# Optimization experiments

Hardware: AMD Instinct MI355X
Metric: run time of the kernel (lower is better)

## Reference

```python
import jax, jax.numpy as jnp
import numpy as np

NEG = -1e9
NP_N, EP = 30000, 480000
NL, EL, T = 48, 144, 96
NA, D = 11, 256
I_STOP = NL
PHI = 1 + 5 * D + 4 * NA
VAL_VEC = jnp.array([4., 1., 3., 1., 2., 1., 5., 1., 6., 1., 1000.], dtype=jnp.float32)
BOND_VAL = jnp.array([1., 2., 3., 1.5], dtype=jnp.float32)


def gcn2(x, src, dst, w, W1, b1, W2, b2):
    # two-layer GCN with symmetric norm + self loops (PyG GCNConv semantics)
    n = x.shape[0]
    loops = jnp.arange(n, dtype=src.dtype)
    s = jnp.concatenate([src, loops])
    d = jnp.concatenate([dst, loops])
    ww = jnp.concatenate([w, jnp.ones((n,), x.dtype)])
    deg = jax.ops.segment_sum(ww, d, num_segments=n)
    dinv = jnp.where(deg > 0, deg ** -0.5, 0.0)
    norm = (ww * dinv[s] * dinv[d])[:, None]
    def conv(h, W, b):
        return jax.ops.segment_sum((h @ W)[s] * norm, d, num_segments=n) + b
    return conv(jax.nn.relu(conv(x, W1, b1)), W2, b2)


def _forward(x_p, x_l_geom, Wp1, bp1, Wp2, bp2, Wl1, bl1, Wl2, bl2,
             Wd1, bd1, Wd2, bd2, Wf, bf, Wg, bg, Wh, bh,
             src_p, dst_p, src_l, dst_l, x_l_label, bfs_index, bfs_bond):
    f32, i32 = jnp.float32, jnp.int32
    src_p = src_p.astype(i32); dst_p = dst_p.astype(i32)
    src_l = src_l.astype(i32); dst_l = dst_l.astype(i32)
    bfs_index = bfs_index.astype(i32); bfs_bond = bfs_bond.astype(i32)
    x_l_label = x_l_label.astype(i32)
    x_l = jnp.concatenate([x_l_geom, jax.nn.one_hot(x_l_label, NA, dtype=f32)], 1)
    z_pocket = gcn2(x_p, src_p, dst_p, jnp.ones((EP,), f32), Wp1, bp1, Wp2, bp2).mean(0)
    z_l = gcn2(x_l, src_l, dst_l, jnp.ones((EL,), f32), Wl1, bl1, Wl2, bl2)
    lab_true = x_l[:, 4:]
    # f: atom label classifier, teacher-forced log prob of true labels
    lmask = jnp.zeros((NA,), f32).at[-1].set(NEG)
    logp = jax.nn.log_softmax(z_l @ Wf + bf + lmask, -1)[jnp.arange(NL), x_l_label].sum()
    H_init = jnp.concatenate([z_l, lab_true], 1).mean(0)
    lab_v = jnp.concatenate([lab_true, jax.nn.one_hot(jnp.array([NA - 1]), NA, dtype=f32)], 0)  # append Stop node
    e0 = bfs_index[0]
    z_v0 = gcn2(lab_v, e0[:1], e0[1:2], jnp.ones((1,), f32), Wd1, bd1, Wd2, bd2)
    H_t0 = jnp.concatenate([z_v0, lab_v], 1).mean(0)
    val0 = lab_v @ VAL_VEC
    N1 = NL + 1
    E = 2 * T
    Q0 = jnp.zeros((T + 1,), i32).at[0].set(bfs_index[0, 0])
    carry0 = (jnp.asarray(0.0, f32), val0, jnp.zeros((N1,), bool), jnp.zeros((N1, N1), bool),
              jnp.zeros((E,), i32), jnp.zeros((E,), i32), jnp.zeros((E,), bool), jnp.asarray(0, i32),
              Q0, jnp.asarray(0, i32), jnp.asarray(1, i32), z_v0, H_t0, jnp.asarray(0.0, f32))

    def step(carry, xs):
        logp, val, closed, adj, esrc, edst, evalid, ec, Q, head, tail, z_v, H_t, time = carry
        v, bidx = xs
        active = tail > head
        u = Q[head]
        phi = jnp.concatenate([
            jnp.full((N1, 1), time, f32),
            jnp.broadcast_to(z_pocket, (N1, D)),
            jnp.broadcast_to(z_v[u], (N1, D)),
            jnp.broadcast_to(lab_v[u], (N1, NA)),
            z_v, lab_v,
            jnp.broadcast_to(H_t, (N1, D + NA)),
            jnp.broadcast_to(H_init, (N1, D + NA))], 1)
        # node mask (valency / closed / already-bonded / self), then unmask {v, stop}
        base = jnp.where((val < 1) | closed | adj[u], NEG, 0.0).at[u].set(NEG)
        m_nou = jnp.where(val[u] < 1, jnp.full((N1,), NEG, f32), base)
        m = m_nou.at[v].set(0.0).at[I_STOP].set(0.0)
        glog = (phi @ Wg + bg)[:, 0] + m
        logp = logp + jnp.where(active, jax.nn.log_softmax(glog)[v], 0.0)
        is_stop = v == I_STOP
        pop = active & is_stop
        do_edge = active & (~is_stop)
        closed = closed.at[u].set(jnp.where(pop, True, closed[u]))
        head = head + pop.astype(jnp.int32)
        Q = Q.at[tail].set(jnp.where(do_edge, v, Q[tail]), mode='drop')
        tail = tail + do_edge.astype(jnp.int32)
        esrc = esrc.at[ec].set(u, mode='drop').at[ec + 1].set(v, mode='drop')
        edst = edst.at[ec].set(v, mode='drop').at[ec + 1].set(u, mode='drop')
        evalid = evalid.at[ec].set(do_edge, mode='drop').at[ec + 1].set(do_edge, mode='drop')
        ec = ec + 2 * do_edge.astype(jnp.int32)
        # bond mask row on min valency of (u, v)
        mv = jnp.minimum(val[u], val[v])
        two = jnp.array([0., 0., NEG, 0.], f32)
        one = jnp.array([0., NEG, NEG, 0.], f32)
        zer = jnp.full((4,), NEG, f32)
        e = jnp.where(mv <= 2, two, jnp.zeros((4,), f32))
        e = jnp.where(mv <= 1, one, e)
        e = jnp.where(mv <= 0, zer, e)
        e = jnp.where(m_nou[v] <= NEG * 0.5, zer, e)
        e = e.at[bidx].set(0.0)  # unmask true bond
        hlog = phi[v] @ Wh + bh + e
        logp = logp + jnp.where(do_edge, jax.nn.log_softmax(hlog)[bidx], 0.0)
        dec = jnp.where(do_edge, BOND_VAL[bidx], 0.0)
        val = val.at[u].add(-dec).at[v].add(-dec)
        adj = adj.at[u, v].set(jnp.where(do_edge, True, adj[u, v])).at[v, u].set(jnp.where(do_edge, True, adj[v, u]))
        z_new = gcn2(lab_v, esrc, edst, evalid.astype(f32), Wd1, bd1, Wd2, bd2)
        z_v = jnp.where(do_edge, z_new, z_v)
        H_t = jnp.where(do_edge, jnp.concatenate([z_new, lab_v], 1).mean(0), H_t)
        time = time + do_edge.astype(f32)
        return (logp, val, closed, adj, esrc, edst, evalid, ec, Q, head, tail, z_v, H_t, time), None

    carry, _ = jax.lax.scan(step, carry0, (bfs_index[:, 1], bfs_bond))
    return carry[0]


def setup_inputs():
    key = jax.random.key(0)
    ks = jax.random.split(key, 30)
    f32 = jnp.float32
    def w(i, shape):
        return jax.random.normal(ks[i], shape, f32) * 0.05
    inp = {}
    inp['x_p'] = jax.random.normal(ks[0], (NP_N, 15), f32)
    inp['src_p'] = jax.random.randint(ks[1], (EP,), 0, NP_N)
    inp['dst_p'] = jax.random.randint(ks[2], (EP,), 0, NP_N)
    inp['x_l_geom'] = jax.random.normal(ks[3], (NL, 4), f32)
    inp['x_l_label'] = jax.random.randint(ks[4], (NL,), 0, NA - 1)
    inp['src_l'] = jax.random.randint(ks[5], (EL,), 0, NL)
    inp['dst_l'] = jax.random.randint(ks[6], (EL,), 0, NL)
    inp['bfs_index'] = jax.random.randint(ks[7], (T, 2), 0, NL + 1)
    inp['bfs_bond'] = jax.random.randint(ks[8], (T,), 0, 4)
    inp['Wp1'] = w(9, (15, D)); inp['bp1'] = w(10, (D,))
    inp['Wp2'] = w(11, (D, D)); inp['bp2'] = w(12, (D,))
    inp['Wl1'] = w(13, (15, D)); inp['bl1'] = w(14, (D,))
    inp['Wl2'] = w(15, (D, D)); inp['bl2'] = w(16, (D,))
    inp['Wd1'] = w(17, (NA, D)); inp['bd1'] = w(18, (D,))
    inp['Wd2'] = w(19, (D, D)); inp['bd2'] = w(20, (D,))
    inp['Wf'] = w(21, (D, NA)); inp['bf'] = w(22, (NA,))
    inp['Wg'] = w(23, (PHI, 1)); inp['bg'] = w(24, (1,))
    inp['Wh'] = w(25, (PHI, 4)); inp['bh'] = w(26, (4,))
    return inp


def reference(x_p, src_p, dst_p, x_l_geom, x_l_label, src_l, dst_l, bfs_index, bfs_bond,
              Wp1, bp1, Wp2, bp2, Wl1, bl1, Wl2, bl2, Wd1, bd1, Wd2, bd2,
              Wf, bf, Wg, bg, Wh, bh):
    return _forward(x_p, x_l_geom, Wp1, bp1, Wp2, bp2, Wl1, bl1, Wl2, bl2,
                    Wd1, bd1, Wd2, bd2, Wf, bf, Wg, bg, Wh, bh,
                    src_p, dst_p, src_l, dst_l, x_l_label, bfs_index, bfs_bond)
```

## Files before the change

kernel.cpp:

```cpp
#include <hip/hip_runtime.h>
#include <math.h>

#define NPn 30000
#define EPn 480000
#define NLl 48
#define ELl 144
#define Tn 96
#define NAn 11
#define Dn 256
#define N1 49
#define NEGf (-1000000000.0f)
#define NSTATES 97
#define CHN 125
#define PC 13
#define YN (N1*PC)


__global__ void k_deg(const int* __restrict__ dst, int* __restrict__ deg){
  int e = blockIdx.x*blockDim.x + threadIdx.x;
  if (e < EPn) atomicAdd(&deg[dst[e]], 1);
}


__global__ __launch_bounds__(256) void k_mega(
    const int* __restrict__ src_p, const int* __restrict__ dst_p, const float* __restrict__ xp,
    const int* __restrict__ deg, float* __restrict__ xagg, float* __restrict__ odegw,
    const int* __restrict__ lab_in, const int* __restrict__ bfs_i, const int* __restrict__ bfs_b,
    int* __restrict__ lab_idx, float* __restrict__ lab_means,
    int* __restrict__ dirs, int* __restrict__ dird, float* __restrict__ m_arr,
    float* __restrict__ e_arr, int* __restrict__ rec, int* __restrict__ Sout,
    const float* __restrict__ xg, const int* __restrict__ srcl, const int* __restrict__ dstl,
    const float* __restrict__ Wl1, const float* __restrict__ bl1,
    const float* __restrict__ Wl2, const float* __restrict__ bl2, float* __restrict__ zl_mean,
    const float* __restrict__ Wd2, const float* __restrict__ Wg, const float* __restrict__ Wh,
    float* __restrict__ Pm){
  const int bid = blockIdx.x;
  const int tid = threadIdx.x;

  if (bid >= 66){
    int g = (bid-66)*256 + tid;
    int e = g>>4, c = g&15;
    if (e >= EPn) return;
    int s = src_p[e], d = dst_p[e];
    if (c < 15){
      float dvs = rsqrtf((float)(deg[s]+1));
      atomicAdd(&xagg[d*16+c], xp[s*15+c]*dvs);
    } else {
      float dvd = rsqrtf((float)(deg[d]+1));
      atomicAdd(&odegw[s], dvd);
    }
    return;
  }

  if (bid == 0){
    __shared__ int sv[Tn], sb[Tn];
    __shared__ int qarr[Tn+1];
    __shared__ int2 ctrl[Tn];
    __shared__ float valuA[Tn], valvA[Tn];
    __shared__ float baseB[Tn][N1];
    __shared__ int slab[N1];
    __shared__ int cntL[NAn];
    if (tid < Tn){ sv[tid]=bfs_i[2*tid+1]; sb[tid]=bfs_b[tid]; }
    if (tid <= Tn) qarr[tid]=0;
    if (tid < NAn) cntL[tid]=0;
    if (tid < N1){ int l=(tid<NLl)? lab_in[tid] : (NAn-1); slab[tid]=l; lab_idx[tid]=l; }
    __syncthreads();
    if (tid < NLl) atomicAdd(&cntL[slab[tid]],1);
    if (tid == 0) qarr[0]=bfs_i[0];
    __syncthreads();
    if (tid < NAn){
      int c=cntL[tid];
      lab_means[tid]     = ((float)c + ((tid==NAn-1)?1.f:0.f))*(1.0f/49.0f);
      lab_means[NAn+tid] = (float)c*(1.0f/48.0f);
    }
    if (tid == 0){
      dirs[192]=qarr[0]; dird[192]=bfs_i[1];
      int head=0, tail=1, ec=0, timec=0;
      for (int t=0;t<Tn;t++){
        int v = sv[t], bix = sb[t];
        int active = (tail>head)?1:0;
        int h = (head<=Tn)? head : Tn;
        int u = qarr[h];
        int is_stop = (v==NLl)?1:0;
        int pop = active & is_stop;
        int doe = active & (is_stop^1);
        ctrl[t] = make_int2(u | (doe<<8) | (pop<<9) | (active<<10) | (timec<<16), v | (bix<<8));
        if (doe){
          if (tail<=Tn) qarr[tail]=v;
          if (ec<192){ dirs[ec]=u; dird[ec]=v; dirs[ec+1]=v; dird[ec+1]=u; }
        }
        head+=pop; tail+=doe; ec+=2*doe; timec+=doe;
      }
      Sout[0]=ec/2;
    }
    __syncthreads();
    if (tid < Tn){
      int2 c=ctrl[tid];
      rec[tid]=c.x&255; rec[Tn+tid]=c.y&255; rec[2*Tn+tid]=(c.y>>8)&3;
      rec[3*Tn+tid]=(c.x>>10)&1; rec[4*Tn+tid]=(c.x>>8)&1; rec[5*Tn+tid]=(c.x>>16)&255;
    }
    __syncthreads();
    if (tid < 64){
      const int l = tid;
      int labv = (l<N1)? slab[l] : (NAn-1);
      float val;
      switch(labv){
        case 0: val=4.f; break; case 1: val=1.f; break; case 2: val=3.f; break;
        case 3: val=1.f; break; case 4: val=2.f; break; case 5: val=1.f; break;
        case 6: val=5.f; break; case 7: val=1.f; break; case 8: val=6.f; break;
        case 9: val=1.f; break; default: val=1000.f; break;
      }
      if (l>=N1) val=0.f;
      int closed=0;
      unsigned long long adjm=0ull;
      #pragma unroll 4
      for (int t=0;t<Tn;t++){
        int2 c=ctrl[t];
        int u=c.x&255, doe=(c.x>>8)&1, pop=(c.x>>9)&1;
        int v=c.y&255, bix=(c.y>>8)&3;
        float base = (val<1.f || closed || ((adjm>>u)&1ull)) ? NEGf : 0.f;
        if (l==u) base=NEGf;
        if (l<N1) baseB[t][l]=base;
        if (l==u) valuA[t]=val;
        if (l==v) valvA[t]=val;
        if (doe){
          float dec = (bix==0)?1.f:(bix==1)?2.f:(bix==2)?3.f:1.5f;
          if (l==u){ val-=dec; adjm |= (1ull<<v); }
          if (l==v){ val-=dec; adjm |= (1ull<<u); }
        }
        if (pop && l==u) closed=1;
      }
    }
    __syncthreads();
    {
      const int lane=tid&63, wv=tid>>6;
      for (int t=wv; t<Tn; t+=4){
        float valu=valuA[t], valv=valvA[t];
        int v=sv[t], bix=sb[t];
        if (lane<N1){
          float mnou = (valu<1.f)? NEGf : baseB[t][lane];
          float m = mnou;
          if (lane==v) m=0.f;
          if (lane==NLl) m=0.f;
          m_arr[t*N1+lane]=m;
        }
        if (lane<4){
          float mnv = (valu<1.f)? NEGf : baseB[t][v];
          float mv = fminf(valu,valv);
          float e;
          if (mv<=0.f) e=NEGf;
          else if (mv<=1.f) e=((lane==1)||(lane==2))?NEGf:0.f;
          else if (mv<=2.f) e=(lane==2)?NEGf:0.f;
          else e=0.f;
          if (mnv <= NEGf*0.5f) e=NEGf;
          if (lane==bix) e=0.f;
          e_arr[t*4+lane]=e;
        }
      }
    }
    return;
  }

  if (bid == 1){
    __shared__ float sW[15*Dn];
    __shared__ __align__(16) float sagg[NLl][16];
    __shared__ float ow[NLl];
    __shared__ float rs[Dn];
    __shared__ float sdinv[NLl];
    __shared__ int sdeg[NLl];
    __shared__ int ses[ELl], sed[ELl];
    __shared__ int slab2[NLl];
    if (tid<NLl){ sdeg[tid]=1; slab2[tid]=lab_in[tid]; }
    for (int i=tid;i<NLl*16;i+=256) sagg[i>>4][i&15]=0.f;
    for (int i=tid;i<15*Dn;i+=256) sW[i]=Wl1[i];
    __syncthreads();
    if (tid<ELl){ ses[tid]=srcl[tid]; sed[tid]=dstl[tid]; atomicAdd(&sdeg[dstl[tid]],1); }
    __syncthreads();
    if (tid<NLl) sdinv[tid]=rsqrtf((float)sdeg[tid]);
    __syncthreads();
    if (tid<NLl){
      float dv=sdinv[tid];
      ow[tid]=dv;
      for (int q=0;q<4;q++) sagg[tid][q]=xg[tid*4+q]*dv;
      sagg[tid][4+slab2[tid]]=dv;
    }
    __syncthreads();
    if (tid<ELl){
      int s=ses[tid], d=sed[tid];
      float dvs=sdinv[s];
      for (int q=0;q<4;q++) atomicAdd(&sagg[d][q], xg[s*4+q]*dvs);
      atomicAdd(&sagg[d][4+slab2[s]], dvs);
      atomicAdd(&ow[s], sdinv[d]);
    }
    __syncthreads();
    {
      int c=tid;
      float wcol[16];
      #pragma unroll
      for (int q=0;q<15;q++) wcol[q]=sW[q*Dn+c];
      wcol[15]=0.f;
      float b=bl1[c];
      float rsum=0.f;
      for (int d=0;d<NLl;d++){
        const float4* ar=(const float4*)sagg[d];
        float4 x0=ar[0],x1=ar[1],x2=ar[2],x3=ar[3];
        float a=0.f;
        a=fmaf(x0.x,wcol[0],a); a=fmaf(x0.y,wcol[1],a); a=fmaf(x0.z,wcol[2],a); a=fmaf(x0.w,wcol[3],a);
        a=fmaf(x1.x,wcol[4],a); a=fmaf(x1.y,wcol[5],a); a=fmaf(x1.z,wcol[6],a); a=fmaf(x1.w,wcol[7],a);
        a=fmaf(x2.x,wcol[8],a); a=fmaf(x2.y,wcol[9],a); a=fmaf(x2.z,wcol[10],a); a=fmaf(x2.w,wcol[11],a);
        a=fmaf(x3.x,wcol[12],a); a=fmaf(x3.y,wcol[13],a); a=fmaf(x3.z,wcol[14],a);
        float h=fmaxf(sdinv[d]*a + b, 0.f);
        rsum = fmaf(sdinv[d]*ow[d], h, rsum);
      }
      rs[c]=rsum*(1.0f/48.0f);
    }
    __syncthreads();
    {
      int c=tid;
      float a=0.f;
      for (int k=0;k<Dn;k++) a=fmaf(rs[k], Wl2[(size_t)k*Dn+c], a);
      zl_mean[c]=a+bl2[c];
    }
    return;
  }

  {
    const int lane = tid&63, wv = tid>>6;
    const int k = (bid-2)*4 + wv;
    float pg=0.f;
    float4 pu=make_float4(0,0,0,0), pv=make_float4(0,0,0,0), ph=make_float4(0,0,0,0);
    for (int q=0;q<4;q++){
      int n = lane + 64*q;
      float w = Wd2[(size_t)k*Dn+n];
      pg = fmaf(w, Wg[524+n], pg);
      float4 a=*(const float4*)&Wh[(size_t)(257+n)*4];
      float4 b=*(const float4*)&Wh[(size_t)(524+n)*4];
      float4 c=*(const float4*)&Wh[(size_t)(791+n)*4];
      pu.x=fmaf(w,a.x,pu.x); pu.y=fmaf(w,a.y,pu.y); pu.z=fmaf(w,a.z,pu.z); pu.w=fmaf(w,a.w,pu.w);
      pv.x=fmaf(w,b.x,pv.x); pv.y=fmaf(w,b.y,pv.y); pv.z=fmaf(w,b.z,pv.z); pv.w=fmaf(w,b.w,pv.w);
      ph.x=fmaf(w,c.x,ph.x); ph.y=fmaf(w,c.y,ph.y); ph.z=fmaf(w,c.z,ph.z); ph.w=fmaf(w,c.w,ph.w);
    }
    for (int off=32; off>0; off>>=1){
      pg += __shfl_xor(pg,off);
      pu.x+=__shfl_xor(pu.x,off); pu.y+=__shfl_xor(pu.y,off); pu.z+=__shfl_xor(pu.z,off); pu.w+=__shfl_xor(pu.w,off);
      pv.x+=__shfl_xor(pv.x,off); pv.y+=__shfl_xor(pv.y,off); pv.z+=__shfl_xor(pv.z,off); pv.w+=__shfl_xor(pv.w,off);
      ph.x+=__shfl_xor(ph.x,off); ph.y+=__shfl_xor(ph.y,off); ph.z+=__shfl_xor(ph.z,off); ph.w+=__shfl_xor(ph.w,off);
    }
    if (lane==0){
      float* o = Pm + k*PC;
      o[0]=pg; o[1]=pu.x; o[2]=pu.y; o[3]=pu.z; o[4]=pu.w;
      o[5]=pv.x; o[6]=pv.y; o[7]=pv.z; o[8]=pv.w;
      o[9]=ph.x; o[10]=ph.y; o[11]=ph.z; o[12]=ph.w;
    }
    return;
  }
}


__global__ __launch_bounds__(256) void k_fuse(const float* __restrict__ xp, const float* __restrict__ xagg,
    const int* __restrict__ deg, const float* __restrict__ odegw,
    const float* __restrict__ Wp1, const float* __restrict__ bp1, float* __restrict__ zr){
  __shared__ float sx[CHN][16];
  __shared__ float sc[CHN];
  int tid = threadIdx.x;
  int base = blockIdx.x*CHN;
  float wcol[15];
  for (int k=0;k<15;k++) wcol[k]=Wp1[k*Dn+tid];
  float b = bp1[tid];
  for (int i=tid;i<CHN*16;i+=256){
    int n = base+(i>>4), c = i&15;
    float v = 0.f;
    if (n<NPn && c<15){
      float dv = rsqrtf((float)(deg[n]+1));
      v = (xagg[n*16+c] + xp[n*15+c]*dv)*dv;
    }
    sx[i>>4][i&15]=v;
  }
  for (int i=tid;i<CHN;i+=256){
    int n = base+i;
    float dv = (n<NPn)? rsqrtf((float)(deg[n]+1)) : 0.f;
    sc[i] = (n<NPn)? dv*(odegw[n]+dv) : 0.f;
  }
  __syncthreads();
  float acc = 0.f;
  int lim = (NPn-base < CHN)? (NPn-base) : CHN;
  for (int i=0;i<lim;i++){
    float d0 = b;
    for (int k=0;k<15;k++) d0 = fmaf(sx[i][k], wcol[k], d0);
    acc = fmaf(sc[i], fmaxf(d0,0.f), acc);
  }
  atomicAdd(&zr[tid], acc);
}


__global__ __launch_bounds__(256) void k_dcp(const int* __restrict__ Sp, const int* __restrict__ dirs,
    const int* __restrict__ dird, const int* __restrict__ lab_idx,
    const float* __restrict__ Wd1, const float* __restrict__ bd1,
    const float* __restrict__ Pm, const int* __restrict__ rec,
    const float* __restrict__ m_arr, const float* __restrict__ e_arr,
    const float* __restrict__ Wg, const float* __restrict__ Wh,
    float* __restrict__ spart){
  int k = blockIdx.x;
  if (k > Sp[0]) return;
  __shared__ float sW[11*Dn];
  __shared__ float sP[Dn*PC];
  __shared__ float hT[Dn*N1];
  __shared__ float cnt[N1*11];
  __shared__ float y1[YN];
  __shared__ float za[YN];
  __shared__ float sdinv[N1];
  __shared__ int sdeg[N1];
  __shared__ int se[192], sd[192];
  __shared__ int slab[N1];
  __shared__ int srec[6*Tn];
  int tid=threadIdx.x;
  int ecnt = (k==0)?1:(2*k);
  int base = (k==0)?192:0;
  if (tid<N1){ sdeg[tid]=1; slab[tid]=lab_idx[tid]; }
  for (int i=tid;i<N1*11;i+=256) cnt[i]=0.f;
  for (int i=tid;i<11*Dn;i+=256) sW[i]=Wd1[i];
  for (int i=tid;i<Dn*PC;i+=256) sP[i]=Pm[i];
  for (int i=tid;i<6*Tn;i+=256) srec[i]=rec[i];
  __syncthreads();
  if (tid<ecnt){ se[tid]=dirs[base+tid]; sd[tid]=dird[base+tid]; atomicAdd(&sdeg[sd[tid]],1); }
  __syncthreads();
  if (tid<N1) sdinv[tid]=rsqrtf((float)sdeg[tid]);
  __syncthreads();
  if (tid<N1) cnt[tid*11+slab[tid]] = sdinv[tid];
  __syncthreads();
  if (tid<ecnt) atomicAdd(&cnt[sd[tid]*11+slab[se[tid]]], sdinv[se[tid]]);
  __syncthreads();
  {
    int c=tid;
    float wreg[11];
    for (int a=0;a<11;a++) wreg[a]=sW[a*Dn+c];
    float b=bd1[c];
    for (int r=0;r<N1;r++){
      float s=0.f;
      for (int a=0;a<11;a++) s=fmaf(cnt[r*11+a], wreg[a], s);
      hT[c*N1+r]=fmaxf(sdinv[r]*s + b, 0.f);
    }
  }
  __syncthreads();
  for (int idx=tid; idx<YN; idx+=256){
    int r=idx/PC, j=idx-r*PC;
    float acc=0.f;
    for (int c=0;c<Dn;c++) acc=fmaf(hT[c*N1+r], sP[c*PC+j], acc);
    y1[idx]=acc;
    za[idx]=sdinv[r]*acc;
  }
  __syncthreads();
  for (int i=tid; i<ecnt*PC; i+=256){
    int e=i/PC, j=i-e*PC;
    atomicAdd(&za[sd[e]*PC+j], sdinv[se[e]]*y1[se[e]*PC+j]);
  }
  __syncthreads();
  for (int idx=tid; idx<YN; idx+=256){
    int r=idx/PC;
    za[idx]=sdinv[r]*za[idx];
  }
  __syncthreads();
  if (tid>=64) return;
  const int lane=tid;
  for (int t=0;t<Tn;t++){
    if (!srec[3*Tn+t] || srec[5*Tn+t]!=k) continue;
    const int u=srec[t], v=srec[Tn+t], doe=srec[4*Tn+t];
    float g = -INFINITY;
    float4 hm = make_float4(0,0,0,0);
    if (lane<N1){
      const float* zrow = za + lane*PC;
      g = zrow[0] + Wg[780+slab[lane]] + m_arr[t*N1+lane];
      hm.x=zrow[9]; hm.y=zrow[10]; hm.z=zrow[11]; hm.w=zrow[12];
    }
    float gv = __shfl(g, v);
    float gM = g;
    for (int off=32; off>0; off>>=1) gM = fmaxf(gM, __shfl_xor(gM, off));
    float ex = (lane<N1)? expf(g-gM) : 0.f;
    float gS = ex;
    for (int off=32; off>0; off>>=1){
      gS += __shfl_xor(gS, off);
      hm.x+=__shfl_xor(hm.x,off); hm.y+=__shfl_xor(hm.y,off);
      hm.z+=__shfl_xor(hm.z,off); hm.w+=__shfl_xor(hm.w,off);
    }
    if (lane==0){
      spart[t*5] = gv - gM - logf(gS);
      if (doe){
        const int lu=slab[u], lv=slab[v];
        const float tf=(float)k;
        for (int j=0;j<4;j++){
          float hmj = (j==0)?hm.x:(j==1)?hm.y:(j==2)?hm.z:hm.w;
          spart[t*5+1+j] = tf*Wh[j] + Wh[(513+lu)*4+j] + Wh[(780+lv)*4+j]
               + za[u*PC+1+j] + za[v*PC+5+j] + hmj*(1.0f/49.0f) + e_arr[4*t+j];
        }
      }
    }
  }
}


__global__ __launch_bounds__(256) void k_final(const float* __restrict__ zr, const float* __restrict__ Wp2,
    const float* __restrict__ bp2, const float* __restrict__ zl, const float* __restrict__ lm,
    const float* __restrict__ b2, const float* __restrict__ Wh, const float* __restrict__ bh,
    const int* __restrict__ rec, const float* __restrict__ spart, float* __restrict__ out){
  __shared__ float sr[Dn];
  __shared__ float zp[Dn];
  __shared__ float hc4s[4];
  __shared__ float red[Tn];
  int tid=threadIdx.x;
  sr[tid]=zr[tid]*(1.0f/30000.0f);
  __syncthreads();
  float a=0.f;
  for (int k=0;k<Dn;k++) a=fmaf(sr[k],Wp2[(size_t)k*Dn+tid],a);
  zp[tid]=a+bp2[tid];
  __syncthreads();
  if (tid<64){
    int lane=tid;
    float4 h=make_float4(0,0,0,0);
    for (int q=0;q<4;q++){
      int n=lane+64*q;
      float4 w1=*(const float4*)&Wh[(size_t)(1+n)*4];
      float4 w2=*(const float4*)&Wh[(size_t)(1058+n)*4];
      float4 wu=*(const float4*)&Wh[(size_t)(257+n)*4];
      float4 wv=*(const float4*)&Wh[(size_t)(524+n)*4];
      float4 wh=*(const float4*)&Wh[(size_t)(791+n)*4];
      float zpn=zp[n], zln=zl[n], bn=b2[n];
      h.x += zpn*w1.x + zln*w2.x + bn*(wu.x+wv.x+wh.x);
      h.y += zpn*w1.y + zln*w2.y + bn*(wu.y+wv.y+wh.y);
      h.z += zpn*w1.z + zln*w2.z + bn*(wu.z+wv.z+wh.z);
      h.w += zpn*w1.w + zln*w2.w + bn*(wu.w+wv.w+wh.w);
    }
    if (lane<NAn){
      float4 wa=*(const float4*)&Wh[(size_t)(1047+lane)*4];
      float4 wb=*(const float4*)&Wh[(size_t)(1314+lane)*4];
      float aa=lm[lane], bb=lm[NAn+lane];
      h.x += aa*wa.x + bb*wb.x; h.y += aa*wa.y + bb*wb.y;
      h.z += aa*wa.z + bb*wb.z; h.w += aa*wa.w + bb*wb.w;
    }
    for (int off=32; off>0; off>>=1){
      h.x+=__shfl_xor(h.x,off); h.y+=__shfl_xor(h.y,off);
      h.z+=__shfl_xor(h.z,off); h.w+=__shfl_xor(h.w,off);
    }
    if (lane==0){
      hc4s[0]=h.x+bh[0]; hc4s[1]=h.y+bh[1]; hc4s[2]=h.z+bh[2]; hc4s[3]=h.w+bh[3];
    }
  }
  __syncthreads();
  if (tid<Tn){
    int t=tid;
    float res=0.f;
    if (rec[3*Tn+t]){
      res = spart[t*5];
      if (rec[4*Tn+t]){
        int bidx = rec[2*Tn+t];
        float h0=spart[t*5+1]+hc4s[0];
        float h1=spart[t*5+2]+hc4s[1];
        float h2=spart[t*5+3]+hc4s[2];
        float h3=spart[t*5+4]+hc4s[3];
        float M=fmaxf(fmaxf(h0,h1),fmaxf(h2,h3));
        float se2=expf(h0-M)+expf(h1-M)+expf(h2-M)+expf(h3-M);
        float hb=(bidx==0)?h0:(bidx==1)?h1:(bidx==2)?h2:h3;
        res += hb - M - logf(se2);
      }
    }
    red[t]=res;
  }
  __syncthreads();
  if (tid==0){
    float s=0.f;
    for (int t=0;t<Tn;t++) s+=red[t];
    out[0]=s;
  }
}


extern "C" void kernel_launch(void* const* d_in, const int* in_sizes, int n_in,
                              void* d_out, int out_size, void* d_ws, size_t ws_size,
                              hipStream_t stream){
  const float* x_p      =(const float*)d_in[0];
  const int*   src_p    =(const int*)d_in[1];
  const int*   dst_p    =(const int*)d_in[2];
  const float* x_l_geom =(const float*)d_in[3];
  const int*   x_l_label=(const int*)d_in[4];
  const int*   src_l    =(const int*)d_in[5];
  const int*   dst_l    =(const int*)d_in[6];
  const int*   bfs_index=(const int*)d_in[7];
  const int*   bfs_bond =(const int*)d_in[8];
  const float* Wp1=(const float*)d_in[9];
  const float* bp1=(const float*)d_in[10];
  const float* Wp2=(const float*)d_in[11];
  const float* bp2=(const float*)d_in[12];
  const float* Wl1=(const float*)d_in[13];
  const float* bl1=(const float*)d_in[14];
  const float* Wl2=(const float*)d_in[15];
  const float* bl2=(const float*)d_in[16];
  const float* Wd1=(const float*)d_in[17];
  const float* bd1=(const float*)d_in[18];
  const float* Wd2=(const float*)d_in[19];
  const float* bd2=(const float*)d_in[20];
  const float* Wg =(const float*)d_in[23];
  const float* Wh =(const float*)d_in[25];
  const float* bh =(const float*)d_in[26];

  char* w=(char*)d_ws;
  size_t off=0;
  auto alloc=[&](size_t bytes)->char*{ char* p=w+off; off=(off+bytes+255)&~((size_t)255); return p; };
  int*   deg    =(int*)alloc((size_t)NPn*4);
  float* odegw  =(float*)alloc((size_t)NPn*4);
  float* xagg   =(float*)alloc((size_t)NPn*16*4);
  float* zr     =(float*)alloc(Dn*4);
  size_t zero_span = off;
  float* zl_mean=(float*)alloc(Dn*4);
  float* Pm     =(float*)alloc(Dn*PC*4);
  float* m_arr  =(float*)alloc((size_t)Tn*N1*4);
  float* e_arr  =(float*)alloc((size_t)Tn*4*4);
  int*   rec    =(int*)alloc((size_t)6*Tn*4);
  int*   dirs   =(int*)alloc(194*4);
  int*   dird   =(int*)alloc(194*4);
  int*   lab_idx=(int*)alloc(N1*4);
  float* lab_means=(float*)alloc(2*NAn*4);
  int*   Sval   =(int*)alloc(4);
  float* spart  =(float*)alloc((size_t)Tn*5*4);
  (void)in_sizes;(void)n_in;(void)ws_size;(void)out_size;

  hipMemsetAsync(d_ws, 0, zero_span, stream);

  k_deg<<<(EPn+255)/256, 256, 0, stream>>>(dst_p, deg);
  k_mega<<<66 + EPn*16/256, 256, 0, stream>>>(
      src_p, dst_p, x_p, deg, xagg, odegw,
      x_l_label, bfs_index, bfs_bond, lab_idx, lab_means, dirs, dird, m_arr, e_arr, rec, Sval,
      x_l_geom, src_l, dst_l, Wl1, bl1, Wl2, bl2, zl_mean,
      Wd2, Wg, Wh, Pm);
  k_dcp<<<NSTATES,256,0,stream>>>(Sval,dirs,dird,lab_idx,Wd1,bd1,Pm,rec,m_arr,e_arr,Wg,Wh,spart);
  k_fuse<<<(NPn+CHN-1)/CHN,256,0,stream>>>(x_p,xagg,deg,odegw,Wp1,bp1,zr);
  k_final<<<1,256,0,stream>>>(zr,Wp2,bp2,zl_mean,lab_means,bd2,Wh,bh,rec,spart,(float*)d_out);
}
```

Baseline: 268.7 us.

## Fuse degree count into mega kernel, merge scatter with DCP, fold Wp2/Wl2 into Wh projections

Removes the separate degree kernel by running the degree atomics in the extra blocks of k_mega. The edge scatter (xagg/odegw) moves into a new kernel together with the per-state DCP blocks, so those two independent jobs run concurrently. The Wp2 and Wl2 matvecs are folded algebraically: Wp2·Wh and Wl2·Wh products are precomputed in k_mega's Pm blocks. k_final and the ligand block then only need the 256-wide mean vectors, which removes two serial 256x256 matvecs from single-block kernels. This cuts one launch and shortens the serial tail, at the cost of heavier mixed-role blocks and a changed floating-point summation order.

```diff
diff --git a/kernel.cpp b/kernel.cpp
--- a/kernel.cpp
+++ b/kernel.cpp
@@ -14,41 +14,26 @@
 #define CHN 125
 #define PC 13
 #define YN (N1*PC)
-
-
-__global__ void k_deg(const int* __restrict__ dst, int* __restrict__ deg){
-  int e = blockIdx.x*blockDim.x + threadIdx.x;
-  if (e < EPn) atomicAdd(&deg[dst[e]], 1);
-}
+#define DEGB ((EPn+255)/256)
 
 
 __global__ __launch_bounds__(256) void k_mega(
-    const int* __restrict__ src_p, const int* __restrict__ dst_p, const float* __restrict__ xp,
-    const int* __restrict__ deg, float* __restrict__ xagg, float* __restrict__ odegw,
+    const int* __restrict__ dst_p, int* __restrict__ deg,
     const int* __restrict__ lab_in, const int* __restrict__ bfs_i, const int* __restrict__ bfs_b,
     int* __restrict__ lab_idx, float* __restrict__ lab_means,
     int* __restrict__ dirs, int* __restrict__ dird, float* __restrict__ m_arr,
     float* __restrict__ e_arr, int* __restrict__ rec, int* __restrict__ Sout,
     const float* __restrict__ xg, const int* __restrict__ srcl, const int* __restrict__ dstl,
-    const float* __restrict__ Wl1, const float* __restrict__ bl1,
-    const float* __restrict__ Wl2, const float* __restrict__ bl2, float* __restrict__ zl_mean,
+    const float* __restrict__ Wl1, const float* __restrict__ bl1, float* __restrict__ rs_g,
     const float* __restrict__ Wd2, const float* __restrict__ Wg, const float* __restrict__ Wh,
-    float* __restrict__ Pm){
+    const float* __restrict__ Wp2, const float* __restrict__ Wl2,
+    float* __restrict__ Pm, float* __restrict__ Qp, float* __restrict__ Ql){
   const int bid = blockIdx.x;
   const int tid = threadIdx.x;
 
   if (bid >= 66){
-    int g = (bid-66)*256 + tid;
-    int e = g>>4, c = g&15;
-    if (e >= EPn) return;
-    int s = src_p[e], d = dst_p[e];
-    if (c < 15){
-      float dvs = rsqrtf((float)(deg[s]+1));
-      atomicAdd(&xagg[d*16+c], xp[s*15+c]*dvs);
-    } else {
-      float dvd = rsqrtf((float)(deg[d]+1));
-      atomicAdd(&odegw[s], dvd);
-    }
+    int e = (bid-66)*256 + tid;
+    if (e < EPn) atomicAdd(&deg[dst_p[e]], 1);
     return;
   }
 
@@ -165,7 +150,6 @@
     __shared__ float sW[15*Dn];
     __shared__ __align__(16) float sagg[NLl][16];
     __shared__ float ow[NLl];
-    __shared__ float rs[Dn];
     __shared__ float sdinv[NLl];
     __shared__ int sdeg[NLl];
     __shared__ int ses[ELl], sed[ELl];
@@ -212,14 +196,7 @@
         float h=fmaxf(sdinv[d]*a + b, 0.f);
         rsum = fmaf(sdinv[d]*ow[d], h, rsum);
       }
-      rs[c]=rsum*(1.0f/48.0f);
-    }
-    __syncthreads();
-    {
-      int c=tid;
-      float a=0.f;
-      for (int k=0;k<Dn;k++) a=fmaf(rs[k], Wl2[(size_t)k*Dn+c], a);
-      zl_mean[c]=a+bl2[c];
+      rs_g[c]=rsum*(1.0f/48.0f);
     }
     return;
   }
@@ -229,6 +206,7 @@
     const int k = (bid-2)*4 + wv;
     float pg=0.f;
     float4 pu=make_float4(0,0,0,0), pv=make_float4(0,0,0,0), ph=make_float4(0,0,0,0);
+    float4 qp=make_float4(0,0,0,0), ql=make_float4(0,0,0,0);
     for (int q=0;q<4;q++){
       int n = lane + 64*q;
       float w = Wd2[(size_t)k*Dn+n];
@@ -239,20 +217,155 @@
       pu.x=fmaf(w,a.x,pu.x); pu.y=fmaf(w,a.y,pu.y); pu.z=fmaf(w,a.z,pu.z); pu.w=fmaf(w,a.w,pu.w);
       pv.x=fmaf(w,b.x,pv.x); pv.y=fmaf(w,b.y,pv.y); pv.z=fmaf(w,b.z,pv.z); pv.w=fmaf(w,b.w,pv.w);
       ph.x=fmaf(w,c.x,ph.x); ph.y=fmaf(w,c.y,ph.y); ph.z=fmaf(w,c.z,ph.z); ph.w=fmaf(w,c.w,ph.w);
+      float wp = Wp2[(size_t)k*Dn+n];
+      float wl = Wl2[(size_t)k*Dn+n];
+      float4 w1=*(const float4*)&Wh[(size_t)(1+n)*4];
+      float4 w2=*(const float4*)&Wh[(size_t)(1058+n)*4];
+      qp.x=fmaf(wp,w1.x,qp.x); qp.y=fmaf(wp,w1.y,qp.y); qp.z=fmaf(wp,w1.z,qp.z); qp.w=fmaf(wp,w1.w,qp.w);
+      ql.x=fmaf(wl,w2.x,ql.x); ql.y=fmaf(wl,w2.y,ql.y); ql.z=fmaf(wl,w2.z,ql.z); ql.w=fmaf(wl,w2.w,ql.w);
     }
     for (int off=32; off>0; off>>=1){
       pg += __shfl_xor(pg,off);
       pu.x+=__shfl_xor(pu.x,off); pu.y+=__shfl_xor(pu.y,off); pu.z+=__shfl_xor(pu.z,off); pu.w+=__shfl_xor(pu.w,off);
       pv.x+=__shfl_xor(pv.x,off); pv.y+=__shfl_xor(pv.y,off); pv.z+=__shfl_xor(pv.z,off); pv.w+=__shfl_xor(pv.w,off);
       ph.x+=__shfl_xor(ph.x,off); ph.y+=__shfl_xor(ph.y,off); ph.z+=__shfl_xor(ph.z,off); ph.w+=__shfl_xor(ph.w,off);
+      qp.x+=__shfl_xor(qp.x,off); qp.y+=__shfl_xor(qp.y,off); qp.z+=__shfl_xor(qp.z,off); qp.w+=__shfl_xor(qp.w,off);
+      ql.x+=__shfl_xor(ql.x,off); ql.y+=__shfl_xor(ql.y,off); ql.z+=__shfl_xor(ql.z,off); ql.w+=__shfl_xor(ql.w,off);
     }
     if (lane==0){
       float* o = Pm + k*PC;
       o[0]=pg; o[1]=pu.x; o[2]=pu.y; o[3]=pu.z; o[4]=pu.w;
       o[5]=pv.x; o[6]=pv.y; o[7]=pv.z; o[8]=pv.w;
       o[9]=ph.x; o[10]=ph.y; o[11]=ph.z; o[12]=ph.w;
+      *(float4*)&Qp[k*4] = qp;
+      *(float4*)&Ql[k*4] = ql;
     }
     return;
+  }
+}
+
+
+__global__ __launch_bounds__(256) void k_dx(
+    const int* __restrict__ src_p, const int* __restrict__ dst_p, const float* __restrict__ xp,
+    const int* __restrict__ deg, float* __restrict__ xagg, float* __restrict__ odegw,
+    const int* __restrict__ Sp, const int* __restrict__ dirs,
+    const int* __restrict__ dird, const int* __restrict__ lab_idx,
+    const float* __restrict__ Wd1, const float* __restrict__ bd1,
+    const float* __restrict__ Pm, const int* __restrict__ rec,
+    const float* __restrict__ m_arr, const float* __restrict__ e_arr,
+    const float* __restrict__ Wg, const float* __restrict__ Wh,
+    float* __restrict__ spart){
+  const int bid = blockIdx.x;
+  const int tid = threadIdx.x;
+
+  if (bid >= NSTATES){
+    int g = (bid-NSTATES)*256 + tid;
+    int e = g>>4, c = g&15;
+    if (e >= EPn) return;
+    int s = src_p[e], d = dst_p[e];
+    if (c < 15){
+      float dvs = rsqrtf((float)(deg[s]+1));
+      atomicAdd(&xagg[d*16+c], xp[s*15+c]*dvs);
+    } else {
+      float dvd = rsqrtf((float)(deg[d]+1));
+      atomicAdd(&odegw[s], dvd);
+    }
+    return;
+  }
+
+  int k = bid;
+  if (k > Sp[0]) return;
+  __shared__ float sW[11*Dn];
+  __shared__ float sP[Dn*PC];
+  __shared__ float hT[Dn*N1];
+  __shared__ float cnt[N1*11];
+  __shared__ float y1[YN];
+  __shared__ float za[YN];
+  __shared__ float sdinv[N1];
+  __shared__ int sdeg[N1];
+  __shared__ int se[192], sd[192];
+  __shared__ int slab[N1];
+  __shared__ int srec[6*Tn];
+  int ecnt = (k==0)?1:(2*k);
+  int base = (k==0)?192:0;
+  if (tid<N1){ sdeg[tid]=1; slab[tid]=lab_idx[tid]; }
+  for (int i=tid;i<N1*11;i+=256) cnt[i]=0.f;
+  for (int i=tid;i<11*Dn;i+=256) sW[i]=Wd1[i];
+  for (int i=tid;i<Dn*PC;i+=256) sP[i]=Pm[i];
+  for (int i=tid;i<6*Tn;i+=256) srec[i]=rec[i];
+  __syncthreads();
+  if (tid<ecnt){ se[tid]=dirs[base+tid]; sd[tid]=dird[base+tid]; atomicAdd(&sdeg[sd[tid]],1); }
+  __syncthreads();
+  if (tid<N1) sdinv[tid]=rsqrtf((float)sdeg[tid]);
+  __syncthreads();
+  if (tid<N1) cnt[tid*11+slab[tid]] = sdinv[tid];
+  __syncthreads();
+  if (tid<ecnt) atomicAdd(&cnt[sd[tid]*11+slab[se[tid]]], sdinv[se[tid]]);
+  __syncthreads();
+  {
+    int c=tid;
+    float wreg[11];
+    for (int a=0;a<11;a++) wreg[a]=sW[a*Dn+c];
+    float b=bd1[c];
+    for (int r=0;r<N1;r++){
+      float s=0.f;
+      for (int a=0;a<11;a++) s=fmaf(cnt[r*11+a], wreg[a], s);
+      hT[c*N1+r]=fmaxf(sdinv[r]*s + b, 0.f);
+    }
+  }
+  __syncthreads();
+  for (int idx=tid; idx<YN; idx+=256){
+    int r=idx/PC, j=idx-r*PC;
+    float acc=0.f;
+    for (int c=0;c<Dn;c++) acc=fmaf(hT[c*N1+r], sP[c*PC+j], acc);
+    y1[idx]=acc;
+    za[idx]=sdinv[r]*acc;
+  }
+  __syncthreads();
+  for (int i=tid; i<ecnt*PC; i+=256){
+    int e=i/PC, j=i-e*PC;
+    atomicAdd(&za[sd[e]*PC+j], sdinv[se[e]]*y1[se[e]*PC+j]);
+  }
+  __syncthreads();
+  for (int idx=tid; idx<YN; idx+=256){
+    int r=idx/PC;
+    za[idx]=sdinv[r]*za[idx];
+  }
+  __syncthreads();
+  if (tid>=64) return;
+  const int lane=tid;
+  for (int t=0;t<Tn;t++){
+    if (!srec[3*Tn+t] || srec[5*Tn+t]!=k) continue;
+    const int u=srec[t], v=srec[Tn+t], doe=srec[4*Tn+t];
+    float g = -INFINITY;
+    float4 hm = make_float4(0,0,0,0);
+    if (lane<N1){
+      const float* zrow = za + lane*PC;
+      g = zrow[0] + Wg[780+slab[lane]] + m_arr[t*N1+lane];
+      hm.x=zrow[9]; hm.y=zrow[10]; hm.z=zrow[11]; hm.w=zrow[12];
+    }
+    float gv = __shfl(g, v);
+    float gM = g;
+    for (int off=32; off>0; off>>=1) gM = fmaxf(gM, __shfl_xor(gM, off));
+    float ex = (lane<N1)? expf(g-gM) : 0.f;
+    float gS = ex;
+    for (int off=32; off>0; off>>=1){
+      gS += __shfl_xor(gS, off);
+      hm.x+=__shfl_xor(hm.x,off); hm.y+=__shfl_xor(hm.y,off);
+      hm.z+=__shfl_xor(hm.z,off); hm.w+=__shfl_xor(hm.w,off);
+    }
+    if (lane==0){
+      spart[t*5] = gv - gM - logf(gS);
+      if (doe){
+        const int lu=slab[u], lv=slab[v];
+        const float tf=(float)k;
+        for (int j=0;j<4;j++){
+          float hmj = (j==0)?hm.x:(j==1)?hm.y:(j==2)?hm.z:hm.w;
+          spart[t*5+1+j] = tf*Wh[j] + Wh[(513+lu)*4+j] + Wh[(780+lv)*4+j]
+               + za[u*PC+1+j] + za[v*PC+5+j] + hmj*(1.0f/49.0f) + e_arr[4*t+j];
+        }
+      }
+    }
   }
 }
 
@@ -293,141 +406,36 @@
 }
 
 
-__global__ __launch_bounds__(256) void k_dcp(const int* __restrict__ Sp, const int* __restrict__ dirs,
-    const int* __restrict__ dird, const int* __restrict__ lab_idx,
-    const float* __restrict__ Wd1, const float* __restrict__ bd1,
-    const float* __restrict__ Pm, const int* __restrict__ rec,
-    const float* __restrict__ m_arr, const float* __restrict__ e_arr,
-    const float* __restrict__ Wg, const float* __restrict__ Wh,
-    float* __restrict__ spart){
-  int k = blockIdx.x;
-  if (k > Sp[0]) return;
-  __shared__ float sW[11*Dn];
-  __shared__ float sP[Dn*PC];
-  __shared__ float hT[Dn*N1];
-  __shared__ float cnt[N1*11];
-  __shared__ float y1[YN];
-  __shared__ float za[YN];
-  __shared__ float sdinv[N1];
-  __shared__ int sdeg[N1];
-  __shared__ int se[192], sd[192];
-  __shared__ int slab[N1];
-  __shared__ int srec[6*Tn];
-  int tid=threadIdx.x;
-  int ecnt = (k==0)?1:(2*k);
-  int base = (k==0)?192:0;
-  if (tid<N1){ sdeg[tid]=1; slab[tid]=lab_idx[tid]; }
-  for (int i=tid;i<N1*11;i+=256) cnt[i]=0.f;
-  for (int i=tid;i<11*Dn;i+=256) sW[i]=Wd1[i];
-  for (int i=tid;i<Dn*PC;i+=256) sP[i]=Pm[i];
-  for (int i=tid;i<6*Tn;i+=256) srec[i]=rec[i];
-  __syncthreads();
-  if (tid<ecnt){ se[tid]=dirs[base+tid]; sd[tid]=dird[base+tid]; atomicAdd(&sdeg[sd[tid]],1); }
-  __syncthreads();
-  if (tid<N1) sdinv[tid]=rsqrtf((float)sdeg[tid]);
-  __syncthreads();
-  if (tid<N1) cnt[tid*11+slab[tid]] = sdinv[tid];
-  __syncthreads();
-  if (tid<ecnt) atomicAdd(&cnt[sd[tid]*11+slab[se[tid]]], sdinv[se[tid]]);
-  __syncthreads();
-  {
-    int c=tid;
-    float wreg[11];
-    for (int a=0;a<11;a++) wreg[a]=sW[a*Dn+c];
-    float b=bd1[c];
-    for (int r=0;r<N1;r++){
-      float s=0.f;
-      for (int a=0;a<11;a++) s=fmaf(cnt[r*11+a], wreg[a], s);
-      hT[c*N1+r]=fmaxf(sdinv[r]*s + b, 0.f);
-    }
-  }
-  __syncthreads();
-  for (int idx=tid; idx<YN; idx+=256){
-    int r=idx/PC, j=idx-r*PC;
-    float acc=0.f;
-    for (int c=0;c<Dn;c++) acc=fmaf(hT[c*N1+r], sP[c*PC+j], acc);
-    y1[idx]=acc;
-    za[idx]=sdinv[r]*acc;
-  }
-  __syncthreads();
-  for (int i=tid; i<ecnt*PC; i+=256){
-    int e=i/PC, j=i-e*PC;
-    atomicAdd(&za[sd[e]*PC+j], sdinv[se[e]]*y1[se[e]*PC+j]);
-  }
-  __syncthreads();
-  for (int idx=tid; idx<YN; idx+=256){
-    int r=idx/PC;
-    za[idx]=sdinv[r]*za[idx];
-  }
-  __syncthreads();
-  if (tid>=64) return;
-  const int lane=tid;
-  for (int t=0;t<Tn;t++){
-    if (!srec[3*Tn+t] || srec[5*Tn+t]!=k) continue;
-    const int u=srec[t], v=srec[Tn+t], doe=srec[4*Tn+t];
-    float g = -INFINITY;
-    float4 hm = make_float4(0,0,0,0);
-    if (lane<N1){
-      const float* zrow = za + lane*PC;
-      g = zrow[0] + Wg[780+slab[lane]] + m_arr[t*N1+lane];
-      hm.x=zrow[9]; hm.y=zrow[10]; hm.z=zrow[11]; hm.w=zrow[12];
-    }
-    float gv = __shfl(g, v);
-    float gM = g;
-    for (int off=32; off>0; off>>=1) gM = fmaxf(gM, __shfl_xor(gM, off));
-    float ex = (lane<N1)? expf(g-gM) : 0.f;
-    float gS = ex;
-    for (int off=32; off>0; off>>=1){
-      gS += __shfl_xor(gS, off);
-      hm.x+=__shfl_xor(hm.x,off); hm.y+=__shfl_xor(hm.y,off);
-      hm.z+=__shfl_xor(hm.z,off); hm.w+=__shfl_xor(hm.w,off);
-    }
-    if (lane==0){
-      spart[t*5] = gv - gM - logf(gS);
-      if (doe){
-        const int lu=slab[u], lv=slab[v];
-        const float tf=(float)k;
-        for (int j=0;j<4;j++){
-          float hmj = (j==0)?hm.x:(j==1)?hm.y:(j==2)?hm.z:hm.w;
-          spart[t*5+1+j] = tf*Wh[j] + Wh[(513+lu)*4+j] + Wh[(780+lv)*4+j]
-               + za[u*PC+1+j] + za[v*PC+5+j] + hmj*(1.0f/49.0f) + e_arr[4*t+j];
-        }
-      }
-    }
-  }
-}
-
-
-__global__ __launch_bounds__(256) void k_final(const float* __restrict__ zr, const float* __restrict__ Wp2,
-    const float* __restrict__ bp2, const float* __restrict__ zl, const float* __restrict__ lm,
-    const float* __restrict__ b2, const float* __restrict__ Wh, const float* __restrict__ bh,
+__global__ __launch_bounds__(256) void k_final(const float* __restrict__ zr, const float* __restrict__ rs_g,
+    const float* __restrict__ Qp, const float* __restrict__ Ql,
+    const float* __restrict__ bp2, const float* __restrict__ bl2, const float* __restrict__ b2,
+    const float* __restrict__ lm, const float* __restrict__ Wh, const float* __restrict__ bh,
     const int* __restrict__ rec, const float* __restrict__ spart, float* __restrict__ out){
   __shared__ float sr[Dn];
-  __shared__ float zp[Dn];
+  __shared__ float rsg[Dn];
   __shared__ float hc4s[4];
   __shared__ float red[Tn];
   int tid=threadIdx.x;
   sr[tid]=zr[tid]*(1.0f/30000.0f);
-  __syncthreads();
-  float a=0.f;
-  for (int k=0;k<Dn;k++) a=fmaf(sr[k],Wp2[(size_t)k*Dn+tid],a);
-  zp[tid]=a+bp2[tid];
+  rsg[tid]=rs_g[tid];
   __syncthreads();
   if (tid<64){
     int lane=tid;
     float4 h=make_float4(0,0,0,0);
     for (int q=0;q<4;q++){
       int n=lane+64*q;
+      float srn=sr[n], rsn=rsg[n], bpn=bp2[n], bln=bl2[n], bdn=b2[n];
+      float4 qp=*(const float4*)&Qp[n*4];
+      float4 ql=*(const float4*)&Ql[n*4];
       float4 w1=*(const float4*)&Wh[(size_t)(1+n)*4];
       float4 w2=*(const float4*)&Wh[(size_t)(1058+n)*4];
       float4 wu=*(const float4*)&Wh[(size_t)(257+n)*4];
       float4 wv=*(const float4*)&Wh[(size_t)(524+n)*4];
       float4 wh=*(const float4*)&Wh[(size_t)(791+n)*4];
-      float zpn=zp[n], zln=zl[n], bn=b2[n];
-      h.x += zpn*w1.x + zln*w2.x + bn*(wu.x+wv.x+wh.x);
-      h.y += zpn*w1.y + zln*w2.y + bn*(wu.y+wv.y+wh.y);
-      h.z += zpn*w1.z + zln*w2.z + bn*(wu.z+wv.z+wh.z);
-      h.w += zpn*w1.w + zln*w2.w + bn*(wu.w+wv.w+wh.w);
+      h.x += srn*qp.x + rsn*ql.x + bpn*w1.x + bln*w2.x + bdn*(wu.x+wv.x+wh.x);
+      h.y += srn*qp.y + rsn*ql.y + bpn*w1.y + bln*w2.y + bdn*(wu.y+wv.y+wh.y);
+      h.z += srn*qp.z + rsn*ql.z + bpn*w1.z + bln*w2.z + bdn*(wu.z+wv.z+wh.z);
+      h.w += srn*qp.w + rsn*ql.w + bpn*w1.w + bln*w2.w + bdn*(wu.w+wv.w+wh.w);
     }
     if (lane<NAn){
       float4 wa=*(const float4*)&Wh[(size_t)(1047+lane)*4];
@@ -509,8 +517,10 @@
   float* xagg   =(float*)alloc((size_t)NPn*16*4);
   float* zr     =(float*)alloc(Dn*4);
   size_t zero_span = off;
-  float* zl_mean=(float*)alloc(Dn*4);
+  float* rs_g   =(float*)alloc(Dn*4);
   float* Pm     =(float*)alloc(Dn*PC*4);
+  float* Qp     =(float*)alloc(Dn*4*4);
+  float* Ql     =(float*)alloc(Dn*4*4);
   float* m_arr  =(float*)alloc((size_t)Tn*N1*4);
   float* e_arr  =(float*)alloc((size_t)Tn*4*4);
   int*   rec    =(int*)alloc((size_t)6*Tn*4);
@@ -524,13 +534,14 @@
 
   hipMemsetAsync(d_ws, 0, zero_span, stream);
 
-  k_deg<<<(EPn+255)/256, 256, 0, stream>>>(dst_p, deg);
-  k_mega<<<66 + EPn*16/256, 256, 0, stream>>>(
+  k_mega<<<66 + DEGB, 256, 0, stream>>>(
+      dst_p, deg,
+      x_l_label, bfs_index, bfs_bond, lab_idx, lab_means, dirs, dird, m_arr, e_arr, rec, Sval,
+      x_l_geom, src_l, dst_l, Wl1, bl1, rs_g,
+      Wd2, Wg, Wh, Wp2, Wl2, Pm, Qp, Ql);
+  k_dx<<<NSTATES + EPn*16/256, 256, 0, stream>>>(
       src_p, dst_p, x_p, deg, xagg, odegw,
-      x_l_label, bfs_index, bfs_bond, lab_idx, lab_means, dirs, dird, m_arr, e_arr, rec, Sval,
-      x_l_geom, src_l, dst_l, Wl1, bl1, Wl2, bl2, zl_mean,
-      Wd2, Wg, Wh, Pm);
-  k_dcp<<<NSTATES,256,0,stream>>>(Sval,dirs,dird,lab_idx,Wd1,bd1,Pm,rec,m_arr,e_arr,Wg,Wh,spart);
+      Sval, dirs, dird, lab_idx, Wd1, bd1, Pm, rec, m_arr, e_arr, Wg, Wh, spart);
   k_fuse<<<(NPn+CHN-1)/CHN,256,0,stream>>>(x_p,xagg,deg,odegw,Wp1,bp1,zr);
-  k_final<<<1,256,0,stream>>>(zr,Wp2,bp2,zl_mean,lab_means,bd2,Wh,bh,rec,spart,(float*)d_out);
+  k_final<<<1,256,0,stream>>>(zr,rs_g,Qp,Ql,bp2,bl2,bd2,lab_means,Wh,bh,rec,spart,(float*)d_out);
 }
```

After: 374.7 us. 39.5% more time.
